# Kernel optimization log

Measured on AMD Instinct MI355X. Metric: run time of the kernel, lower is better.

## Reference

```python
import jax, jax.numpy as jnp
import numpy as np

N_NODES = 50000
N_EDGES = 800000
IN_F = 128
OUT_F = 128
HEADS = 8
HEAD_DIM = OUT_F // HEADS
EDGE_F = 32


def setup_inputs() -> dict:
    key = jax.random.key(0)
    ks = jax.random.split(key, 14)
    s = lambda fan_in: 1.0 / np.sqrt(fan_in)
    return {
        "node_features": jax.random.normal(ks[0], (N_NODES, IN_F), jnp.float32),
        "edge_index": jax.random.randint(ks[1], (2, N_EDGES), 0, N_NODES, jnp.int64),
        "edge_features": jax.random.normal(ks[2], (N_EDGES, EDGE_F), jnp.float32),
        "Wq": jax.random.uniform(ks[3], (IN_F, OUT_F), jnp.float32, -s(IN_F), s(IN_F)),
        "bq": jnp.zeros((OUT_F,), jnp.float32),
        "Wk": jax.random.uniform(ks[4], (IN_F, OUT_F), jnp.float32, -s(IN_F), s(IN_F)),
        "bk": jnp.zeros((OUT_F,), jnp.float32),
        "Wv": jax.random.uniform(ks[5], (IN_F, OUT_F), jnp.float32, -s(IN_F), s(IN_F)),
        "bv": jnp.zeros((OUT_F,), jnp.float32),
        "We": jax.random.uniform(ks[6], (EDGE_F, HEADS), jnp.float32, -s(EDGE_F), s(EDGE_F)),
        "be": jnp.zeros((HEADS,), jnp.float32),
        "Wo": jax.random.uniform(ks[7], (OUT_F, OUT_F), jnp.float32, -s(OUT_F), s(OUT_F)),
        "bo": jnp.zeros((OUT_F,), jnp.float32),
    }


def reference(node_features, edge_index, edge_features,
              Wq, bq, Wk, bk, Wv, bv, We, be, Wo, bo):
    n_nodes = node_features.shape[0]
    n_edges = edge_index.shape[1]
    sources, targets = edge_index[0], edge_index[1]
    scale = HEAD_DIM ** -0.5

    # dense projections: [n_nodes, heads, head_dim]
    Q = (node_features @ Wq + bq).reshape(n_nodes, HEADS, HEAD_DIM)
    K = (node_features @ Wk + bk).reshape(n_nodes, HEADS, HEAD_DIM)
    V = (node_features @ Wv + bv).reshape(n_nodes, HEADS, HEAD_DIM)

    # gather by edge
    Q_t = Q[targets]           # [n_edges, heads, head_dim]
    K_s = K[sources]
    V_s = V[sources]

    scores = jnp.sum(Q_t * K_s, axis=-1) * scale      # [n_edges, heads]
    scores = scores + (edge_features @ We + be)       # edge bias

    # segment softmax over incoming edges of each target node
    max_s = jax.ops.segment_max(scores, targets, num_segments=n_nodes)
    scores = scores - max_s[targets]
    exp_s = jnp.exp(scores)
    denom = jax.ops.segment_sum(exp_s, targets, num_segments=n_nodes) + 1e-10
    probs = exp_s / denom[targets]                    # [n_edges, heads]

    weighted_V = probs[:, :, None] * V_s              # [n_edges, heads, head_dim]
    aggregated = jax.ops.segment_sum(
        weighted_V.reshape(n_edges, -1), targets, num_segments=n_nodes)
    return aggregated @ Wo + bo
```

## Files before the change

kernel.cpp:

```cpp
#include <hip/hip_runtime.h>

typedef __attribute__((ext_vector_type(8))) short shortx8;
typedef __attribute__((ext_vector_type(4))) float floatx4;
typedef unsigned short u16;
typedef unsigned int u32;

__device__ __forceinline__ float bf2f(unsigned short u) {
    union { unsigned int i; float f; } v; v.i = ((unsigned int)u) << 16; return v.f;
}
__device__ __forceinline__ float bfl(u32 u) {
    union { u32 i; float f; } v; v.i = u << 16; return v.f;
}
__device__ __forceinline__ float bfh(u32 u) {
    union { u32 i; float f; } v; v.i = u & 0xFFFF0000u; return v.f;
}
__device__ __forceinline__ unsigned short f2bf(float f) {
    union { float f; unsigned int i; } v; v.f = f;
    unsigned int x = v.i;
    unsigned int r = x + 0x7FFFu + ((x >> 16) & 1u);
    return (unsigned short)(r >> 16);
}
__device__ __forceinline__ u32 pack2bf(float a, float b) {
    return (u32)f2bf(a) | ((u32)f2bf(b) << 16);
}
__device__ __forceinline__ float ldf(const void* p, int i, bool f32) {
    return f32 ? ((const float*)p)[i] : bf2f(((const u16*)p)[i]);
}

__global__ __launch_bounds__(256) void prep_all_k(
    const u16* __restrict__ nf, const int* __restrict__ ei,
    const void* __restrict__ W0, const void* __restrict__ W1,
    const void* __restrict__ W2, const void* __restrict__ W3,
    const void* __restrict__ b0, const void* __restrict__ b1,
    const void* __restrict__ b2, const void* __restrict__ b3,
    const void* __restrict__ We, const void* __restrict__ be,
    int* __restrict__ flags, int* __restrict__ deg,
    u16* __restrict__ WT, float* __restrict__ biasWs,
    float* __restrict__ WeWs, float* __restrict__ beWs, int M)
{
    int tid = threadIdx.x;
    int bid = blockIdx.x;
    if (bid >= 33) {
        int i = (bid - 33) * 256 + tid;
        if (i < M) deg[i] = 0;
        return;
    }
    __shared__ int cnt[2];
    if (tid < 2) cnt[tid] = 0;
    __syncthreads();
    int c0 = 0;
    for (int i = tid; i < 8192; i += 256) {
        u16 v = nf[i];
        if ((v & 0x7F80u) == 0x7F80u) c0++;
    }
    atomicAdd(&cnt[0], c0);
    if (bid == 32) {
        int c1 = 0;
        for (int i = tid; i < 1024; i += 256) {
            if (ei[2 * i + 1] != 0) c1++;
        }
        atomicAdd(&cnt[1], c1);
    }
    __syncthreads();
    bool f32 = cnt[0] > 6;

    if (bid < 32) {
        int t = bid * 256 + tid;
        int mat  = t >> 11;
        int r    = t & 2047;
        int lane = r & 63;
        int ks   = (r >> 6) & 3;
        int ct   = r >> 8;
        const void* W = (mat == 0) ? W0 : (mat == 1) ? W1 : (mat == 2) ? W2 : W3;
        int k0  = ks * 32 + (lane >> 4) * 8;
        int col = ct * 16 + (lane & 15);
        u16 tmp[8];
#pragma unroll
        for (int j = 0; j < 8; ++j) {
            int off = (k0 + j) * 128 + col;
            tmp[j] = f32 ? f2bf(((const float*)W)[off]) : ((const u16*)W)[off];
        }
        *(shortx8*)(WT + (size_t)t * 8) = *(const shortx8*)tmp;
    } else {
        if (tid == 0) {
            flags[0] = f32 ? 1 : 0;
            flags[1] = (cnt[1] < 100) ? 1 : 0;
        }
        if (tid < 128) {
            biasWs[0 * 128 + tid] = ldf(b0, tid, f32);
            biasWs[1 * 128 + tid] = ldf(b1, tid, f32);
            biasWs[2 * 128 + tid] = ldf(b2, tid, f32);
            biasWs[3 * 128 + tid] = ldf(b3, tid, f32);
        }
        WeWs[tid] = ldf(We, tid, f32);
        if (tid < 8) beWs[tid] = ldf(be, tid, f32);
    }
}

__global__ __launch_bounds__(256) void hist_rank_k(
    const int* __restrict__ ei, int* __restrict__ deg, int* __restrict__ rank,
    int E, const int* __restrict__ flags)
{
    int e = blockIdx.x * 256 + threadIdx.x;
    if (e >= E) return;
    int tgt = flags[1] ? ei[2 * (E + e)] : ei[E + e];
    rank[e] = atomicAdd(&deg[tgt], 1);
}

__global__ __launch_bounds__(256) void scan1_k(
    const int* __restrict__ deg, int* __restrict__ incl, int* __restrict__ bsum, int M)
{
    __shared__ int s[256];
    int tid = threadIdx.x;
    int i = blockIdx.x * 256 + tid;
    int v = (i < M) ? deg[i] : 0;
    s[tid] = v;
    __syncthreads();
#pragma unroll
    for (int off = 1; off < 256; off <<= 1) {
        int t = (tid >= off) ? s[tid - off] : 0;
        __syncthreads();
        s[tid] += t;
        __syncthreads();
    }
    if (i < M) incl[i] = s[tid];
    if (tid == 255) bsum[blockIdx.x] = s[255];
}

__global__ __launch_bounds__(256) void scan23_k(
    const int* __restrict__ bsum, const int* __restrict__ incl,
    int* __restrict__ rowptr, int M, int nb)
{
    __shared__ int s[256];
    int tid = threadIdx.x;
    int v = (tid < nb) ? bsum[tid] : 0;
    s[tid] = v;
    __syncthreads();
#pragma unroll
    for (int off = 1; off < 256; off <<= 1) {
        int t = (tid >= off) ? s[tid - off] : 0;
        __syncthreads();
        s[tid] += t;
        __syncthreads();
    }
    int b = blockIdx.x;
    int boffb = (b == 0) ? 0 : s[b - 1];
    int i = b * 256 + tid;
    if (i >= M) return;
    rowptr[i + 1] = incl[i] + boffb;
    if (i == 0) rowptr[0] = 0;
}

__global__ __launch_bounds__(256) void qkv_gemm_k(
    const void* __restrict__ A, int M,
    const u16* __restrict__ WT, const float* __restrict__ biasWs,
    u16* __restrict__ Qb, u16* __restrict__ KVb,
    const int* __restrict__ flags)
{
    bool aF32 = flags[0] != 0;
    int lane = threadIdx.x & 63;
    int wave = threadIdx.x >> 6;
    int quad = lane >> 4;
    int l15  = lane & 15;
    int m0   = blockIdx.x * 128 + wave * 32;

    shortx8 afrag[2][4];
#pragma unroll
    for (int mt = 0; mt < 2; ++mt) {
        int row = m0 + mt * 16 + l15;
        row = row < M ? row : M - 1;
#pragma unroll
        for (int ks = 0; ks < 4; ++ks) {
            size_t base = (size_t)row * 128 + ks * 32 + quad * 8;
            if (aF32) {
                const floatx4* ap = (const floatx4*)((const float*)A + base);
                floatx4 f0 = ap[0], f1 = ap[1];
                u16 tmp[8];
#pragma unroll
                for (int j = 0; j < 4; ++j) { tmp[j] = f2bf(f0[j]); tmp[4 + j] = f2bf(f1[j]); }
                afrag[mt][ks] = *(const shortx8*)tmp;
            } else {
                afrag[mt][ks] = *(const shortx8*)((const u16*)A + base);
            }
        }
    }

#pragma unroll
    for (int mat = 0; mat < 3; ++mat) {
        floatx4 acc[2][8];
#pragma unroll
        for (int a = 0; a < 2; ++a)
#pragma unroll
            for (int b = 0; b < 8; ++b)
                acc[a][b] = (floatx4){0.f, 0.f, 0.f, 0.f};
#pragma unroll
        for (int ks = 0; ks < 4; ++ks) {
#pragma unroll
            for (int ct = 0; ct < 8; ++ct) {
                shortx8 bfrag = *(const shortx8*)(WT + (size_t)mat * 16384 +
                                                  ((size_t)(ct * 4 + ks) * 64 + lane) * 8);
                acc[0][ct] = __builtin_amdgcn_mfma_f32_16x16x32_bf16(afrag[0][ks], bfrag, acc[0][ct], 0, 0, 0);
                acc[1][ct] = __builtin_amdgcn_mfma_f32_16x16x32_bf16(afrag[1][ks], bfrag, acc[1][ct], 0, 0, 0);
            }
        }
        u16* base = (mat == 0) ? Qb : (mat == 1) ? KVb : (KVb + 128);
        int stride = (mat == 0) ? 128 : 256;
#pragma unroll
        for (int ct = 0; ct < 8; ++ct) {
            int col = ct * 16 + l15;
            float bs = biasWs[mat * 128 + col];
#pragma unroll
            for (int mt = 0; mt < 2; ++mt) {
#pragma unroll
                for (int r = 0; r < 4; ++r) {
                    int row = m0 + mt * 16 + quad * 4 + r;
                    if (row < M)
                        base[(size_t)row * stride + col] = f2bf(acc[mt][ct][r] + bs);
                }
            }
        }
    }
}

__global__ __launch_bounds__(256) void scatter_eb_k(
    const int* __restrict__ ei, const void* __restrict__ ef,
    const int* __restrict__ rank, const int* __restrict__ rowptr,
    const float* __restrict__ WeWs, const float* __restrict__ beWs,
    uint4* __restrict__ rec, int E, const int* __restrict__ flags)
{
    __shared__ float sWe[256];
    __shared__ float sbe[8];
    int tid = threadIdx.x;
    sWe[tid] = WeWs[tid];
    if (tid < 8) sbe[tid] = beWs[tid];
    __syncthreads();

    int e = blockIdx.x * 256 + tid;
    if (e >= E) return;
    bool f32 = flags[0] != 0;
    bool i64 = flags[1] != 0;

    int src = i64 ? ei[2 * e]       : ei[e];
    int tgt = i64 ? ei[2 * (E + e)] : ei[E + e];
    int pos = rowptr[tgt] + rank[e];

    float v[32];
    if (f32) {
        const floatx4* ep = (const floatx4*)((const float*)ef + (size_t)e * 32);
#pragma unroll
        for (int g = 0; g < 8; ++g) {
            floatx4 t = ep[g];
#pragma unroll
            for (int j = 0; j < 4; ++j) v[g * 4 + j] = t[j];
        }
    } else {
        const shortx8* ep = (const shortx8*)((const u16*)ef + (size_t)e * 32);
#pragma unroll
        for (int g = 0; g < 4; ++g) {
            shortx8 t = ep[g];
#pragma unroll
            for (int j = 0; j < 8; ++j) v[g * 8 + j] = bf2f((unsigned short)t[j]);
        }
    }
    float eb[8];
#pragma unroll
    for (int h = 0; h < 8; ++h) eb[h] = sbe[h];
#pragma unroll
    for (int k = 0; k < 32; ++k)
#pragma unroll
        for (int h = 0; h < 8; ++h) eb[h] += v[k] * sWe[k * 8 + h];

    uint4 r0, r1;
    r0.x = (u32)src;
    r0.y = pack2bf(eb[0], eb[1]);
    r0.z = pack2bf(eb[2], eb[3]);
    r0.w = pack2bf(eb[4], eb[5]);
    r1.x = pack2bf(eb[6], eb[7]);
    r1.y = 0; r1.z = 0; r1.w = 0;
    rec[(size_t)pos * 2]     = r0;
    rec[(size_t)pos * 2 + 1] = r1;
}

__global__ __launch_bounds__(256) void node_agg_k(
    const uint4* __restrict__ rec, const int* __restrict__ rowptr,
    const u16* __restrict__ Qb, const u16* __restrict__ KVb,
    u16* __restrict__ aggN, int M, int E)
{
    int wave = threadIdx.x >> 6;
    int lane = threadIdx.x & 63;
    int n = blockIdx.x * 4 + wave;
    if (n >= M) return;
    int g = lane >> 4;
    int w = lane & 15;
    int h = w >> 1;

    int beg = rowptr[n], end = rowptr[n + 1];
    int ridx = beg + (lane >> 1);
    if (ridx >= E) ridx = E - 1;
    uint4 pv = rec[(size_t)ridx * 2 + (lane & 1)];

    uint4 qw = ((const uint4*)(Qb + (size_t)n * 128))[w];
    float q0 = bfl(qw.x), q1 = bfh(qw.x), q2 = bfl(qw.y), q3 = bfh(qw.y);
    float q4 = bfl(qw.z), q5 = bfh(qw.z), q6 = bfl(qw.w), q7 = bfh(qw.w);

    float acc[8];
#pragma unroll
    for (int j = 0; j < 8; ++j) acc[j] = 0.f;
    float dsum = 0.f;

    for (int i = beg; i < end; i += 8) {
        int idxA = i + g;
        int idxB = i + 4 + g;
        bool vA = idxA < end;
        bool vB = idxB < end;
        int cA = vA ? idxA : (end - 1);
        int cB = vB ? idxB : (end - 1);
        int offA = cA - beg;
        int offB = cB - beg;

        int srcA, srcB;
        float ebA, ebB;
        if (offA < 32) {
            srcA = __shfl((int)pv.x, 2 * offA);
            u32 w01 = __shfl((int)pv.y, 2 * offA);
            u32 w23 = __shfl((int)pv.z, 2 * offA);
            u32 w45 = __shfl((int)pv.w, 2 * offA);
            u32 w67 = __shfl((int)pv.x, 2 * offA + 1);
            u32 sel = (h < 2) ? w01 : (h < 4) ? w23 : (h < 6) ? w45 : w67;
            ebA = (h & 1) ? bfh(sel) : bfl(sel);
        } else {
            const u32* rw = (const u32*)(rec + (size_t)cA * 2);
            srcA = (int)rw[0];
            u32 sel = rw[1 + h / 2];
            ebA = (h & 1) ? bfh(sel) : bfl(sel);
        }
        if (offB < 32) {
            srcB = __shfl((int)pv.x, 2 * offB);
            u32 w01 = __shfl((int)pv.y, 2 * offB);
            u32 w23 = __shfl((int)pv.z, 2 * offB);
            u32 w45 = __shfl((int)pv.w, 2 * offB);
            u32 w67 = __shfl((int)pv.x, 2 * offB + 1);
            u32 sel = (h < 2) ? w01 : (h < 4) ? w23 : (h < 6) ? w45 : w67;
            ebB = (h & 1) ? bfh(sel) : bfl(sel);
        } else {
            const u32* rw = (const u32*)(rec + (size_t)cB * 2);
            srcB = (int)rw[0];
            u32 sel = rw[1 + h / 2];
            ebB = (h & 1) ? bfh(sel) : bfl(sel);
        }

        const uint4* kpA = (const uint4*)(KVb + (size_t)srcA * 256);
        const uint4* kpB = (const uint4*)(KVb + (size_t)srcB * 256);
        uint4 kwA = kpA[w];
        uint4 kwB = kpB[w];
        uint4 vwA = kpA[16 + w];
        uint4 vwB = kpB[16 + w];

        float partA = q0 * bfl(kwA.x) + q1 * bfh(kwA.x)
                    + q2 * bfl(kwA.y) + q3 * bfh(kwA.y)
                    + q4 * bfl(kwA.z) + q5 * bfh(kwA.z)
                    + q6 * bfl(kwA.w) + q7 * bfh(kwA.w);
        float partB = q0 * bfl(kwB.x) + q1 * bfh(kwB.x)
                    + q2 * bfl(kwB.y) + q3 * bfh(kwB.y)
                    + q4 * bfl(kwB.z) + q5 * bfh(kwB.z)
                    + q6 * bfl(kwB.w) + q7 * bfh(kwB.w);
        partA += __shfl_xor(partA, 1);
        partB += __shfl_xor(partB, 1);
        float pA = vA ? __expf(partA * 0.25f + ebA) : 0.f;
        float pB = vB ? __expf(partB * 0.25f + ebB) : 0.f;
        dsum += pA + pB;
        acc[0] += pA * bfl(vwA.x) + pB * bfl(vwB.x);
        acc[1] += pA * bfh(vwA.x) + pB * bfh(vwB.x);
        acc[2] += pA * bfl(vwA.y) + pB * bfl(vwB.y);
        acc[3] += pA * bfh(vwA.y) + pB * bfh(vwB.y);
        acc[4] += pA * bfl(vwA.z) + pB * bfl(vwB.z);
        acc[5] += pA * bfh(vwA.z) + pB * bfh(vwB.z);
        acc[6] += pA * bfl(vwA.w) + pB * bfl(vwB.w);
        acc[7] += pA * bfh(vwA.w) + pB * bfh(vwB.w);
    }

    dsum += __shfl_xor(dsum, 16);
    dsum += __shfl_xor(dsum, 32);
#pragma unroll
    for (int j = 0; j < 8; ++j) {
        acc[j] += __shfl_xor(acc[j], 16);
        acc[j] += __shfl_xor(acc[j], 32);
    }
    if (g == 0) {
        float inv = 1.0f / (dsum + 1e-10f);
        uint4 o;
        o.x = (u32)f2bf(acc[0] * inv) | ((u32)f2bf(acc[1] * inv) << 16);
        o.y = (u32)f2bf(acc[2] * inv) | ((u32)f2bf(acc[3] * inv) << 16);
        o.z = (u32)f2bf(acc[4] * inv) | ((u32)f2bf(acc[5] * inv) << 16);
        o.w = (u32)f2bf(acc[6] * inv) | ((u32)f2bf(acc[7] * inv) << 16);
        ((uint4*)(aggN + (size_t)n * 128))[w] = o;
    }
}

__global__ __launch_bounds__(256) void out_gemm_k(
    const u16* __restrict__ A, int M,
    const u16* __restrict__ WT, const float* __restrict__ bias,
    void* __restrict__ out, const int* __restrict__ flags)
{
    bool oF32 = flags[0] != 0;
    int lane = threadIdx.x & 63;
    int wave = threadIdx.x >> 6;
    int quad = lane >> 4;
    int l15  = lane & 15;
    int m0   = blockIdx.x * 128 + wave * 32;

    floatx4 acc[2][8];
#pragma unroll
    for (int a = 0; a < 2; ++a)
#pragma unroll
        for (int b = 0; b < 8; ++b)
            acc[a][b] = (floatx4){0.f, 0.f, 0.f, 0.f};

#pragma unroll
    for (int ks = 0; ks < 4; ++ks) {
        shortx8 afrag[2];
#pragma unroll
        for (int mt = 0; mt < 2; ++mt) {
            int row = m0 + mt * 16 + l15;
            row = row < M ? row : M - 1;
            afrag[mt] = *(const shortx8*)(A + (size_t)row * 128 + ks * 32 + quad * 8);
        }
#pragma unroll
        for (int ct = 0; ct < 8; ++ct) {
            shortx8 bfrag = *(const shortx8*)(WT + ((size_t)(ct * 4 + ks) * 64 + lane) * 8);
            acc[0][ct] = __builtin_amdgcn_mfma_f32_16x16x32_bf16(afrag[0], bfrag, acc[0][ct], 0, 0, 0);
            acc[1][ct] = __builtin_amdgcn_mfma_f32_16x16x32_bf16(afrag[1], bfrag, acc[1][ct], 0, 0, 0);
        }
    }

#pragma unroll
    for (int ct = 0; ct < 8; ++ct) {
        int col = ct * 16 + l15;
        float bs = bias[col];
#pragma unroll
        for (int mt = 0; mt < 2; ++mt) {
#pragma unroll
            for (int r = 0; r < 4; ++r) {
                int row = m0 + mt * 16 + quad * 4 + r;
                if (row < M) {
                    float v = acc[mt][ct][r] + bs;
                    if (oF32) ((float*)out)[(size_t)row * 128 + col] = v;
                    else      ((u16*)out)[(size_t)row * 128 + col] = f2bf(v);
                }
            }
        }
    }
}

extern "C" void kernel_launch(void* const* d_in, const int* in_sizes, int n_in,
                              void* d_out, int out_size, void* d_ws, size_t ws_size,
                              hipStream_t stream)
{
    const void* nf = d_in[0];
    const int*  ei = (const int*)d_in[1];
    const void* ef = d_in[2];
    const void* Wq = d_in[3];  const void* bq = d_in[4];
    const void* Wk = d_in[5];  const void* bk = d_in[6];
    const void* Wv = d_in[7];  const void* bv = d_in[8];
    const void* We = d_in[9];  const void* be = d_in[10];
    const void* Wo = d_in[11]; const void* bo = d_in[12];

    int M = in_sizes[0] / 128;
    int E = in_sizes[1] / 2;
    int nb = (M + 255) / 256;

    char* ws = (char*)d_ws;
    int*   flags  = (int*)(ws + 0);
    float* biasWs = (float*)(ws + 256);
    float* WeWs   = (float*)(ws + 2304);
    float* beWs   = (float*)(ws + 3328);
    u16*   WT     = (u16*)(ws + 4096);
    size_t O1 = 4096 + 131072;
    size_t qrow  = (size_t)M * 128 * 2;
    size_t kvrow = (size_t)M * 256 * 2;
    u16* Qb  = (u16*)(ws + O1);
    u16* KVb = (u16*)(ws + O1 + qrow);
    size_t O2 = O1 + qrow + kvrow;
    uint4* rec = (uint4*)(ws + O2);
    size_t O3 = O2 + (size_t)E * 32;
    int* rank   = (int*)(ws + O3);
    int* deg    = rank + E;
    int* incl   = deg + M;
    int* rowptr = incl + M;
    int* bsum   = rowptr + M + 1;
    u16* aggN   = Qb;

    prep_all_k<<<33 + nb, 256, 0, stream>>>((const u16*)nf, ei,
                                            Wq, Wk, Wv, Wo, bq, bk, bv, bo, We, be,
                                            flags, deg, WT, biasWs, WeWs, beWs, M);

    int eblocks = (E + 255) / 256;
    hist_rank_k<<<eblocks, 256, 0, stream>>>(ei, deg, rank, E, flags);
    scan1_k<<<nb, 256, 0, stream>>>(deg, incl, bsum, M);
    scan23_k<<<nb, 256, 0, stream>>>(bsum, incl, rowptr, M, nb);

    int gblocks = (M + 127) / 128;
    qkv_gemm_k<<<gblocks, 256, 0, stream>>>(nf, M, WT, biasWs, Qb, KVb, flags);

    scatter_eb_k<<<eblocks, 256, 0, stream>>>(ei, ef, rank, rowptr, WeWs, beWs,
                                              rec, E, flags);

    node_agg_k<<<(M + 3) / 4, 256, 0, stream>>>(rec, rowptr, Qb, KVb, aggN, M, E);

    out_gemm_k<<<gblocks, 256, 0, stream>>>(aggN, M, WT + 3 * 16384, biasWs + 384, d_out, flags);
}
```

Before: 391.9 us.

## Fuse QKV GEMM with edge scatter and batch four edges per histogram thread

The QKV projection GEMM and the edge-bias scatter kernel are merged into one launch, with block index choosing the role, so the two independent jobs can share the GPU at once and one launch is dropped. The GEMM tile shrinks to 64 rows per block, giving more blocks for that half. The histogram/rank kernel now handles four edges per thread so several loads and atomics are in flight per thread. The out-GEMM grid is rewritten to match the new block-count variable. Risks: the smaller GEMM tile loads each weight fragment for fewer rows, and the mixed launch gives the two halves unequal block durations.

```diff
diff --git a/kernel.cpp b/kernel.cpp
--- a/kernel.cpp
+++ b/kernel.cpp
@@ -101,10 +101,24 @@
     const int* __restrict__ ei, int* __restrict__ deg, int* __restrict__ rank,
     int E, const int* __restrict__ flags)
 {
-    int e = blockIdx.x * 256 + threadIdx.x;
-    if (e >= E) return;
-    int tgt = flags[1] ? ei[2 * (E + e)] : ei[E + e];
-    rank[e] = atomicAdd(&deg[tgt], 1);
+    bool i64 = flags[1] != 0;
+    int base = blockIdx.x * 1024 + threadIdx.x;
+    int e0 = base, e1 = base + 256, e2 = base + 512, e3 = base + 768;
+    bool h0 = e0 < E, h1 = e1 < E, h2 = e2 < E, h3 = e3 < E;
+    int c0 = h0 ? e0 : 0, c1 = h1 ? e1 : 0, c2 = h2 ? e2 : 0, c3 = h3 ? e3 : 0;
+    int t0 = i64 ? ei[2 * (E + c0)] : ei[E + c0];
+    int t1 = i64 ? ei[2 * (E + c1)] : ei[E + c1];
+    int t2 = i64 ? ei[2 * (E + c2)] : ei[E + c2];
+    int t3 = i64 ? ei[2 * (E + c3)] : ei[E + c3];
+    int r0 = 0, r1 = 0, r2 = 0, r3 = 0;
+    if (h0) r0 = atomicAdd(&deg[t0], 1);
+    if (h1) r1 = atomicAdd(&deg[t1], 1);
+    if (h2) r2 = atomicAdd(&deg[t2], 1);
+    if (h3) r3 = atomicAdd(&deg[t3], 1);
+    if (h0) rank[e0] = r0;
+    if (h1) rank[e1] = r1;
+    if (h2) rank[e2] = r2;
+    if (h3) rank[e3] = r3;
 }
 
 __global__ __launch_bounds__(256) void scan1_k(
@@ -151,134 +165,124 @@
     if (i == 0) rowptr[0] = 0;
 }
 
-__global__ __launch_bounds__(256) void qkv_gemm_k(
+__global__ __launch_bounds__(256) void qkv_scatter_k(
     const void* __restrict__ A, int M,
     const u16* __restrict__ WT, const float* __restrict__ biasWs,
     u16* __restrict__ Qb, u16* __restrict__ KVb,
-    const int* __restrict__ flags)
-{
-    bool aF32 = flags[0] != 0;
-    int lane = threadIdx.x & 63;
-    int wave = threadIdx.x >> 6;
-    int quad = lane >> 4;
-    int l15  = lane & 15;
-    int m0   = blockIdx.x * 128 + wave * 32;
-
-    shortx8 afrag[2][4];
-#pragma unroll
-    for (int mt = 0; mt < 2; ++mt) {
-        int row = m0 + mt * 16 + l15;
-        row = row < M ? row : M - 1;
+    const int* __restrict__ ei, const void* __restrict__ ef,
+    const int* __restrict__ rank, const int* __restrict__ rowptr,
+    const float* __restrict__ WeWs, const float* __restrict__ beWs,
+    uint4* __restrict__ rec, int E,
+    const int* __restrict__ flags, int gblocks)
+{
+    __shared__ float sWe[256];
+    __shared__ float sbe[8];
+    bool f32 = flags[0] != 0;
+
+    if (blockIdx.x < gblocks) {
+        int lane = threadIdx.x & 63;
+        int wave = threadIdx.x >> 6;
+        int quad = lane >> 4;
+        int l15  = lane & 15;
+        int m0   = blockIdx.x * 64 + wave * 16;
+
+        shortx8 afrag[4];
 #pragma unroll
         for (int ks = 0; ks < 4; ++ks) {
+            int row = m0 + l15;
+            row = row < M ? row : M - 1;
             size_t base = (size_t)row * 128 + ks * 32 + quad * 8;
-            if (aF32) {
+            if (f32) {
                 const floatx4* ap = (const floatx4*)((const float*)A + base);
                 floatx4 f0 = ap[0], f1 = ap[1];
                 u16 tmp[8];
 #pragma unroll
                 for (int j = 0; j < 4; ++j) { tmp[j] = f2bf(f0[j]); tmp[4 + j] = f2bf(f1[j]); }
-                afrag[mt][ks] = *(const shortx8*)tmp;
+                afrag[ks] = *(const shortx8*)tmp;
             } else {
-                afrag[mt][ks] = *(const shortx8*)((const u16*)A + base);
+                afrag[ks] = *(const shortx8*)((const u16*)A + base);
             }
         }
-    }
-
-#pragma unroll
-    for (int mat = 0; mat < 3; ++mat) {
-        floatx4 acc[2][8];
-#pragma unroll
-        for (int a = 0; a < 2; ++a)
+
+#pragma unroll
+        for (int mat = 0; mat < 3; ++mat) {
+            floatx4 acc[8];
 #pragma unroll
             for (int b = 0; b < 8; ++b)
-                acc[a][b] = (floatx4){0.f, 0.f, 0.f, 0.f};
-#pragma unroll
-        for (int ks = 0; ks < 4; ++ks) {
-#pragma unroll
-            for (int ct = 0; ct < 8; ++ct) {
-                shortx8 bfrag = *(const shortx8*)(WT + (size_t)mat * 16384 +
-                                                  ((size_t)(ct * 4 + ks) * 64 + lane) * 8);
-                acc[0][ct] = __builtin_amdgcn_mfma_f32_16x16x32_bf16(afrag[0][ks], bfrag, acc[0][ct], 0, 0, 0);
-                acc[1][ct] = __builtin_amdgcn_mfma_f32_16x16x32_bf16(afrag[1][ks], bfrag, acc[1][ct], 0, 0, 0);
-            }
-        }
-        u16* base = (mat == 0) ? Qb : (mat == 1) ? KVb : (KVb + 128);
-        int stride = (mat == 0) ? 128 : 256;
-#pragma unroll
-        for (int ct = 0; ct < 8; ++ct) {
-            int col = ct * 16 + l15;
-            float bs = biasWs[mat * 128 + col];
-#pragma unroll
-            for (int mt = 0; mt < 2; ++mt) {
-#pragma unroll
-                for (int r = 0; r < 4; ++r) {
-                    int row = m0 + mt * 16 + quad * 4 + r;
-                    if (row < M)
-                        base[(size_t)row * stride + col] = f2bf(acc[mt][ct][r] + bs);
+                acc[b] = (floatx4){0.f, 0.f, 0.f, 0.f};
+#pragma unroll
+            for (int ks = 0; ks < 4; ++ks) {
+#pragma unroll
+                for (int ct = 0; ct < 8; ++ct) {
+                    shortx8 bfrag = *(const shortx8*)(WT + (size_t)mat * 16384 +
+                                                      ((size_t)(ct * 4 + ks) * 64 + lane) * 8);
+                    acc[ct] = __builtin_amdgcn_mfma_f32_16x16x32_bf16(afrag[ks], bfrag, acc[ct], 0, 0, 0);
                 }
             }
-        }
-    }
-}
-
-__global__ __launch_bounds__(256) void scatter_eb_k(
-    const int* __restrict__ ei, const void* __restrict__ ef,
-    const int* __restrict__ rank, const int* __restrict__ rowptr,
-    const float* __restrict__ WeWs, const float* __restrict__ beWs,
-    uint4* __restrict__ rec, int E, const int* __restrict__ flags)
-{
-    __shared__ float sWe[256];
-    __shared__ float sbe[8];
-    int tid = threadIdx.x;
-    sWe[tid] = WeWs[tid];
-    if (tid < 8) sbe[tid] = beWs[tid];
-    __syncthreads();
-
-    int e = blockIdx.x * 256 + tid;
-    if (e >= E) return;
-    bool f32 = flags[0] != 0;
-    bool i64 = flags[1] != 0;
-
-    int src = i64 ? ei[2 * e]       : ei[e];
-    int tgt = i64 ? ei[2 * (E + e)] : ei[E + e];
-    int pos = rowptr[tgt] + rank[e];
-
-    float v[32];
-    if (f32) {
-        const floatx4* ep = (const floatx4*)((const float*)ef + (size_t)e * 32);
-#pragma unroll
-        for (int g = 0; g < 8; ++g) {
-            floatx4 t = ep[g];
-#pragma unroll
-            for (int j = 0; j < 4; ++j) v[g * 4 + j] = t[j];
+            u16* base = (mat == 0) ? Qb : (mat == 1) ? KVb : (KVb + 128);
+            int stride = (mat == 0) ? 128 : 256;
+#pragma unroll
+            for (int ct = 0; ct < 8; ++ct) {
+                int col = ct * 16 + l15;
+                float bs = biasWs[mat * 128 + col];
+#pragma unroll
+                for (int r = 0; r < 4; ++r) {
+                    int row = m0 + quad * 4 + r;
+                    if (row < M)
+                        base[(size_t)row * stride + col] = f2bf(acc[ct][r] + bs);
+                }
+            }
         }
     } else {
-        const shortx8* ep = (const shortx8*)((const u16*)ef + (size_t)e * 32);
-#pragma unroll
-        for (int g = 0; g < 4; ++g) {
-            shortx8 t = ep[g];
-#pragma unroll
-            for (int j = 0; j < 8; ++j) v[g * 8 + j] = bf2f((unsigned short)t[j]);
-        }
-    }
-    float eb[8];
-#pragma unroll
-    for (int h = 0; h < 8; ++h) eb[h] = sbe[h];
-#pragma unroll
-    for (int k = 0; k < 32; ++k)
-#pragma unroll
-        for (int h = 0; h < 8; ++h) eb[h] += v[k] * sWe[k * 8 + h];
-
-    uint4 r0, r1;
-    r0.x = (u32)src;
-    r0.y = pack2bf(eb[0], eb[1]);
-    r0.z = pack2bf(eb[2], eb[3]);
-    r0.w = pack2bf(eb[4], eb[5]);
-    r1.x = pack2bf(eb[6], eb[7]);
-    r1.y = 0; r1.z = 0; r1.w = 0;
-    rec[(size_t)pos * 2]     = r0;
-    rec[(size_t)pos * 2 + 1] = r1;
+        int tid = threadIdx.x;
+        sWe[tid] = WeWs[tid];
+        if (tid < 8) sbe[tid] = beWs[tid];
+        __syncthreads();
+
+        int e = (blockIdx.x - gblocks) * 256 + tid;
+        if (e >= E) return;
+        bool i64 = flags[1] != 0;
+
+        int src = i64 ? ei[2 * e]       : ei[e];
+        int tgt = i64 ? ei[2 * (E + e)] : ei[E + e];
+        int pos = rowptr[tgt] + rank[e];
+
+        float v[32];
+        if (f32) {
+            const floatx4* ep = (const floatx4*)((const float*)ef + (size_t)e * 32);
+#pragma unroll
+            for (int g = 0; g < 8; ++g) {
+                floatx4 t = ep[g];
+#pragma unroll
+                for (int j = 0; j < 4; ++j) v[g * 4 + j] = t[j];
+            }
+        } else {
+            const shortx8* ep = (const shortx8*)((const u16*)ef + (size_t)e * 32);
+#pragma unroll
+            for (int g = 0; g < 4; ++g) {
+                shortx8 t = ep[g];
+#pragma unroll
+                for (int j = 0; j < 8; ++j) v[g * 8 + j] = bf2f((unsigned short)t[j]);
+            }
+        }
+        float eb[8];
+#pragma unroll
+        for (int h = 0; h < 8; ++h) eb[h] = sbe[h];
+#pragma unroll
+        for (int k = 0; k < 32; ++k)
+#pragma unroll
+            for (int h = 0; h < 8; ++h) eb[h] += v[k] * sWe[k * 8 + h];
+
+        uint4 r0, r1;
+        r0.x = (u32)src;
+        r0.y = pack2bf(eb[0], eb[1]);
+        r0.z = pack2bf(eb[2], eb[3]);
+        r0.w = pack2bf(eb[4], eb[5]);
+        r1.x = pack2bf(eb[6], eb[7]);
+        r1.y = 0; r1.z = 0; r1.w = 0;
+        rec[(size_t)pos * 2]     = r0;
+        rec[(size_t)pos * 2 + 1] = r1;
+    }
 }
 
 __global__ __launch_bounds__(256) void node_agg_k(
@@ -494,18 +498,18 @@
                                             Wq, Wk, Wv, Wo, bq, bk, bv, bo, We, be,
                                             flags, deg, WT, biasWs, WeWs, beWs, M);
 
-    int eblocks = (E + 255) / 256;
-    hist_rank_k<<<eblocks, 256, 0, stream>>>(ei, deg, rank, E, flags);
+    int hblocks = (E + 1023) / 1024;
+    hist_rank_k<<<hblocks, 256, 0, stream>>>(ei, deg, rank, E, flags);
     scan1_k<<<nb, 256, 0, stream>>>(deg, incl, bsum, M);
     scan23_k<<<nb, 256, 0, stream>>>(bsum, incl, rowptr, M, nb);
 
-    int gblocks = (M + 127) / 128;
-    qkv_gemm_k<<<gblocks, 256, 0, stream>>>(nf, M, WT, biasWs, Qb, KVb, flags);
-
-    scatter_eb_k<<<eblocks, 256, 0, stream>>>(ei, ef, rank, rowptr, WeWs, beWs,
-                                              rec, E, flags);
+    int gblocks = (M + 63) / 64;
+    int sblocks = (E + 255) / 256;
+    qkv_scatter_k<<<gblocks + sblocks, 256, 0, stream>>>(
+        nf, M, WT, biasWs, Qb, KVb,
+        ei, ef, rank, rowptr, WeWs, beWs, rec, E, flags, gblocks);
 
     node_agg_k<<<(M + 3) / 4, 256, 0, stream>>>(rec, rowptr, Qb, KVb, aggN, M, E);
 
-    out_gemm_k<<<gblocks, 256, 0, stream>>>(aggN, M, WT + 3 * 16384, biasWs + 384, d_out, flags);
-}
+    out_gemm_k<<<gblocks / 2 + 1, 256, 0, stream>>>(aggN, M, WT + 3 * 16384, biasWs + 384, d_out, flags);
+}
```

Result: no change. 389.8 us (-0.5%).
